# Kernel tuning notes

Hardware: AMD Instinct MI355X
Metric: run time of the kernel (lower is better)

The kernel has to match this reference:

```python
import jax, jax.numpy as jnp
import numpy as np

T, H = 8192, 2048          # num_tokens, hidden_size
NH, NKV, D = 16, 4, 128    # num_heads, num_kv_heads, head_dim
R = 16                     # gate_low_rank_dim
NORM = 16.0                # gate_logit_normalizer
EPS = 1e-6                 # RMSNorm eps


def setup_inputs() -> dict:
    key = jax.random.key(0)
    ks = jax.random.split(key, 8)
    rnd = lambda k, sh, f: jax.random.normal(k, sh, dtype=jnp.float32) * f
    return {
        "hidden_states": rnd(ks[0], (T, H), 1.0),
        "Wqkv": rnd(ks[1], (H, (NH + 2 * NKV) * D), 0.02),
        "bqkv": rnd(ks[2], ((NH + 2 * NKV) * D,), 0.02),
        "gk_w0": rnd(ks[3], (H, R), 0.02),
        "gk_w1": rnd(ks[4], (R, NKV * D), 0.02),
        "gk_b1": rnd(ks[5], (NKV * D,), 0.02),
        "gnorm_w": jnp.ones((D,), jnp.float32),
        "Wo": rnd(ks[6], (NH * D, H), 0.02),
    }


def _gla_scan(q, k, v, g):
    # q,k,v,g: [NH, T, D]. State S: [D, D] per head.
    def step(S, x):
        qt, kt, vt, gt = x
        S = jnp.exp(gt)[:, None] * S + kt[:, None] * vt[None, :]
        return S, qt @ S

    def per_head(qh, kh, vh, gh):
        S0 = jnp.zeros((D, D), qh.dtype)
        _, o = jax.lax.scan(step, S0, (qh, kh, vh, gh))
        return o  # [T, D]

    return jax.vmap(per_head)(q, k, v, g)  # [NH, T, D]


def reference(hidden_states, Wqkv, bqkv, gk_w0, gk_w1, gk_b1, gnorm_w, Wo):
    # qkv projection (with bias), split into q / k / v
    qkv = hidden_states @ Wqkv + bqkv                    # [T, (NH+2*NKV)*D]
    q, k, v = jnp.split(qkv, [NH * D, NH * D + NKV * D], axis=-1)
    # low-rank gate projection (bias0=False, bias1=True)
    gk = (hidden_states @ gk_w0) @ gk_w1 + gk_b1         # [T, NKV*D]

    q = jax.nn.relu(q).reshape(T, NH, D)                 # feature_map = relu
    k = jax.nn.relu(k).reshape(T, NKV, D)
    v = v.reshape(T, NKV, D)
    gk = jax.nn.log_sigmoid(gk).reshape(T, NKV, D) / NORM

    # GQA: repeat_interleave kv heads to NH heads
    rep = NH // NKV
    k = jnp.repeat(k, rep, axis=1)
    v = jnp.repeat(v, rep, axis=1)
    gk = jnp.repeat(gk, rep, axis=1)

    q = q * (D ** -0.5)                                  # fused_chunk_gla default scale

    qh, kh, vh, gh = (t.transpose(1, 0, 2) for t in (q, k, v, gk))  # [NH, T, D]
    o = _gla_scan(qh, kh, vh, gh)                        # [NH, T, D]

    # per-head RMSNorm over head_dim
    o = o * jax.lax.rsqrt(jnp.mean(o * o, axis=-1, keepdims=True) + EPS) * gnorm_w

    o = o.transpose(1, 0, 2).reshape(T, NH * D)          # h n d -> n (h d)
    return o @ Wo                                        # o_proj (no bias)
```

## Files before the change

kernel.cpp:

```cpp
#include <hip/hip_runtime.h>
#include <hip/hip_bf16.h>
#include <cstdint>

typedef unsigned short u16;
typedef unsigned int u32;
typedef float f32x4 __attribute__((ext_vector_type(4)));
typedef short bf16x8 __attribute__((ext_vector_type(8)));

#define T_TOK 8192
#define HID 2048
#define NH 16
#define NKV 4
#define HD 128
#define QKVN 3072
#define CHUNK 64
#define NC 128

__device__ __forceinline__ float bf2f(u16 h){
  u32 u = ((u32)h) << 16;
  return __builtin_bit_cast(float, u);
}
__device__ __forceinline__ u16 f2bf(float f){
  u32 u = __builtin_bit_cast(u32, f);
  u32 r = (u + 0x7fffu + ((u >> 16) & 1u)) >> 16;
  return (u16)r;
}
__device__ __forceinline__ u32 pack2(float a, float b){
  return (u32)f2bf(a) | ((u32)f2bf(b) << 16);
}
__device__ __forceinline__ void gl2lds16(const u16* g, u16* l){
  __builtin_amdgcn_global_load_lds(
      (const __attribute__((address_space(1))) u32*)g,
      (__attribute__((address_space(3))) u32*)l, 16, 0, 0);
}

__global__ __launch_bounds__(256) void cvt_f2b_kernel(
    const float* __restrict__ in, u16* __restrict__ out, int n8)
{
  int i = blockIdx.x*256 + threadIdx.x;
  if (i >= n8) return;
  const float4* p = (const float4*)(in + (size_t)i*8);
  float4 a = p[0], b = p[1];
  uint4 pk;
  pk.x = pack2(a.x, a.y); pk.y = pack2(a.z, a.w);
  pk.z = pack2(b.x, b.y); pk.w = pack2(b.z, b.w);
  *(uint4*)(out + (size_t)i*8) = pk;
}

template<typename YT>
__global__ __launch_bounds__(256) void gemm_m97(
    const u16* __restrict__ X, const u16* __restrict__ Wt,
    const float* __restrict__ bias, const float* __restrict__ ebuf,
    const float* __restrict__ rbuf, YT* __restrict__ Y,
    int M, int N, int K, int mode)
{
  __shared__ u16 As[128*32];
  __shared__ u16 Bs[128*32];
  const int tid = threadIdx.x;
  const int lane = tid & 63;
  const int wave = tid >> 6;
  const int wm = wave >> 1, wn = wave & 1;
  const int bm0 = blockIdx.x * 128, bn0 = blockIdx.y * 128;

  f32x4 acc[4][4];
  #pragma unroll
  for (int i=0;i<4;i++)
    #pragma unroll
    for (int j=0;j<4;j++) acc[i][j] = f32x4{0.f,0.f,0.f,0.f};

  const int row0 = tid >> 2, part8 = (tid & 3) * 8;
  const int mrow = lane & 15, q8 = (lane >> 4) << 3;
  const u16* xb = X  + (size_t)bm0 * K;
  const u16* wb = Wt + (size_t)bn0 * K;

  for (int k0 = 0; k0 < K; k0 += 32) {
    #pragma unroll
    for (int j=0;j<2;j++){
      int rr = j*64 + row0;
      gl2lds16(xb + (size_t)rr*K + k0 + part8, As + rr*32 + part8);
      gl2lds16(wb + (size_t)rr*K + k0 + part8, Bs + rr*32 + part8);
    }
    __syncthreads();
    bf16x8 af[4], bfr[4];
    #pragma unroll
    for (int i=0;i<4;i++){
      af[i]  = *(const bf16x8*)(As + (wm*64 + i*16 + mrow)*32 + q8);
      bfr[i] = *(const bf16x8*)(Bs + (wn*64 + i*16 + mrow)*32 + q8);
    }
    #pragma unroll
    for (int i=0;i<4;i++)
      #pragma unroll
      for (int j=0;j<4;j++)
        acc[i][j] = __builtin_amdgcn_mfma_f32_16x16x32_bf16(af[i], bfr[j], acc[i][j], 0, 0, 0);
    __syncthreads();
  }
  #pragma unroll
  for (int i=0;i<4;i++){
    int row = bm0 + wm*64 + i*16 + (lane>>4)*4;
    #pragma unroll
    for (int j=0;j<4;j++){
      int col = bn0 + wn*64 + j*16 + (lane&15);
      float bv = 0.f;
      if (mode == 1) bv = bias[col];
      #pragma unroll
      for (int rr2=0;rr2<4;rr2++){
        float v = acc[i][j][rr2] + bv;
        if (mode == 1){
          int token = row + rr2;
          int cc = token >> 6, tt = token & 63, ii = col & 127;
          if (col < 2048){
            v = fmaxf(v, 0.f) * 0.08838834764831845f;
            v *= ebuf[(((size_t)cc*4 + (col>>9))*64 + tt)*128 + ii];
          } else if (col < 2560){
            v = fmaxf(v, 0.f);
            v *= rbuf[(((size_t)cc*4 + ((col-2048)>>7))*64 + tt)*128 + ii];
          }
        }
        if (sizeof(YT) == 2) Y[(size_t)(row+rr2)*N + col] = (YT)f2bf(v);
        else                 Y[(size_t)(row+rr2)*N + col] = (YT)v;
      }
    }
  }
}

__global__ __launch_bounds__(256) void transpose_f2b(
    const float* __restrict__ in, u16* __restrict__ out, int R, int C)
{
  __shared__ float tile[32][33];
  int c0 = blockIdx.x*32, r0 = blockIdx.y*32;
  int tx = threadIdx.x & 31, ty = threadIdx.x >> 5;
  #pragma unroll
  for (int p=0;p<4;p++) tile[ty + p*8][tx] = in[(size_t)(r0 + ty + p*8)*C + c0 + tx];
  __syncthreads();
  #pragma unroll
  for (int p=0;p<4;p++) out[(size_t)(c0 + ty + p*8)*R + r0 + tx] = f2bf(tile[tx][ty + p*8]);
}

__global__ __launch_bounds__(256) void gk1_kernel(
    const u16* __restrict__ hsb, const float* __restrict__ w0, float* __restrict__ tmp)
{
  int row = blockIdx.x*4 + (threadIdx.x >> 6);
  int lane = threadIdx.x & 63;
  float acc[16];
  #pragma unroll
  for (int n=0;n<16;n++) acc[n]=0.f;
  for (int k = lane; k < HID; k += 64){
    float h = bf2f(hsb[(size_t)row*HID + k]);
    const float* wr = w0 + (size_t)k*16;
    #pragma unroll
    for (int q=0;q<4;q++){
      float4 wv = *(const float4*)(wr + q*4);
      acc[q*4+0] += h*wv.x; acc[q*4+1] += h*wv.y;
      acc[q*4+2] += h*wv.z; acc[q*4+3] += h*wv.w;
    }
  }
  #pragma unroll
  for (int n=0;n<16;n++){
    #pragma unroll
    for (int off=32; off>0; off>>=1)
      acc[n] += __shfl_down(acc[n], off);
  }
  if (lane == 0){
    #pragma unroll
    for (int n=0;n<16;n++) tmp[(size_t)row*16 + n] = acc[n];
  }
}

__global__ __launch_bounds__(256) void gk2_kernel(
    const float* __restrict__ tmp, const float* __restrict__ w1,
    const float* __restrict__ b1, float* __restrict__ g)
{
  int id = blockIdx.x*256 + threadIdx.x;
  int rrow = id >> 9, n = id & 511;
  float a = b1[n];
  #pragma unroll
  for (int k=0;k<16;k++)
    a += tmp[(size_t)rrow*16 + k] * w1[k*512 + n];
  float ls = fminf(a, 0.f) - log1pf(__expf(-fabsf(a)));
  g[id] = ls * 0.0625f;
}

__global__ __launch_bounds__(256) void decay_kernel(
    const float* __restrict__ g, float* __restrict__ ebuf,
    float* __restrict__ rbuf, float* __restrict__ expB)
{
  __shared__ float bL[CHUNK*HD];
  const int c = blockIdx.x, h = blockIdx.y, tid = threadIdx.x;
  for (int off = tid; off < CHUNK*HD; off += 256){
    int t = off >> 7, i = off & 127;
    bL[off] = g[(size_t)(c*CHUNK + t)*512 + h*HD + i];
  }
  __syncthreads();
  if (tid < HD){
    float run = 0.f;
    for (int t=0;t<CHUNK;t++){ run += bL[t*HD + tid]; bL[t*HD + tid] = run; }
    expB[(size_t)(c*NKV + h)*HD + tid] = __expf(run);
  }
  __syncthreads();
  size_t base = (size_t)(c*NKV + h)*CHUNK*HD;
  for (int off = tid; off < CHUNK*HD; off += 256){
    float b = bL[off];
    ebuf[base + off] = __expf(b);
    rbuf[base + off] = __expf(-b);
  }
}

__global__ __launch_bounds__(256) void chunk_stats2_kernel(
    const u16* __restrict__ qkv, const float* __restrict__ expB,
    u16* __restrict__ Kt, u16* __restrict__ Vt)
{
  __shared__ u16 kL[CHUNK*HD];
  __shared__ u16 vL[CHUNK*HD];
  const int c = blockIdx.x, h = blockIdx.y, tid = threadIdx.x;
  #pragma unroll
  for (int it=0; it<4; it++){
    int u = it*256 + tid;
    int t = u >> 4, p = (u & 15)*8;
    size_t tok = (size_t)(c*CHUNK + t);
    *(uint4*)(kL + t*HD + p) = *(const uint4*)(qkv + tok*QKVN + 2048 + h*HD + p);
    *(uint4*)(vL + t*HD + p) = *(const uint4*)(qkv + tok*QKVN + 2560 + h*HD + p);
  }
  __syncthreads();
  {
    int j = tid >> 1, sh = (tid & 1)*32;
    u16* dst = Vt + ((size_t)(c*NKV + h)*HD + j)*CHUNK + sh;
    #pragma unroll
    for (int s2=0; s2<16; s2++){
      u32 a = (u32)vL[(sh + 2*s2)*HD + j] | ((u32)vL[(sh + 2*s2 + 1)*HD + j] << 16);
      *(u32*)(dst + 2*s2) = a;
    }
  }
  int jj = tid >> 1, ih = (tid & 1)*64;
  float acc[64];
  #pragma unroll
  for (int z=0;z<64;z++) acc[z]=0.f;
  for (int t=0;t<CHUNK;t++){
    float vj = bf2f(vL[t*HD + jj]);
    const u32* kp = (const u32*)(kL + t*HD + ih);
    #pragma unroll
    for (int z2=0; z2<32; z2++){
      u32 kw = kp[z2];
      acc[2*z2]   += vj * bf2f((u16)(kw & 0xffffu));
      acc[2*z2+1] += vj * bf2f((u16)(kw >> 16));
    }
  }
  u16* kout = Kt + ((size_t)(c*NKV + h)*HD + jj)*HD + ih;
  const float* eB = expB + (size_t)(c*NKV + h)*HD + ih;
  #pragma unroll
  for (int z2=0; z2<32; z2++)
    *(u32*)(kout + 2*z2) = pack2(acc[2*z2]*eB[2*z2], acc[2*z2+1]*eB[2*z2+1]);
}

__global__ __launch_bounds__(256) void state_scan2_kernel(
    const u16* __restrict__ Kt, const float* __restrict__ expB, u16* __restrict__ St)
{
  int wid = blockIdx.x;
  int h = wid >> 6;
  int j = (wid & 63)*2 + (threadIdx.x >> 7);
  int i = threadIdx.x & 127;
  size_t base = ((size_t)h*HD + j)*HD + i;
  float S = 0.f;
  for (int cc=0; cc<NC; cc++){
    size_t off = (size_t)cc*(NKV*HD*HD) + base;
    St[off] = f2bf(S);
    S = expB[((size_t)cc*NKV + h)*HD + i] * S + bf2f(Kt[off]);
  }
}

__global__ __launch_bounds__(256) void attn_fused_kernel(
    const u16* __restrict__ qkv, const u16* __restrict__ St,
    const u16* __restrict__ Vt, const float* __restrict__ gw,
    u16* __restrict__ obuf)
{
  __shared__ u16 qe[64*136];
  __shared__ u16 kb[64*136];
  __shared__ u16 sb[64*136];
  __shared__ u16 vb[128*72];
  __shared__ u16 pb[64*72];
  const int c = blockIdx.x, qh = blockIdx.y, h = qh >> 2;
  const int tid = threadIdx.x, lane = tid & 63, w = tid >> 6;
  const int ml = lane & 15, quad = lane >> 4, q8 = quad * 8;

  #pragma unroll
  for (int it = 0; it < 4; it++){
    int u = it*256 + tid;
    int t = u >> 4, p = (u & 15) * 8;
    size_t tok = (size_t)(c*CHUNK + t);
    *(uint4*)(qe + t*136 + p) = *(const uint4*)(qkv + tok*QKVN + qh*HD + p);
    *(uint4*)(kb + t*136 + p) = *(const uint4*)(qkv + tok*QKVN + 2048 + h*HD + p);
  }
  __syncthreads();

  bf16x8 aq[4];
  #pragma unroll
  for (int kk=0;kk<4;kk++)
    aq[kk] = *(const bf16x8*)(qe + (w*16 + ml)*136 + kk*32 + q8);
  #pragma unroll
  for (int n=0;n<4;n++){
    f32x4 pa = {0.f,0.f,0.f,0.f};
    #pragma unroll
    for (int kk=0;kk<4;kk++){
      bf16x8 bk = *(const bf16x8*)(kb + (n*16 + ml)*136 + kk*32 + q8);
      pa = __builtin_amdgcn_mfma_f32_16x16x32_bf16(aq[kk], bk, pa, 0, 0, 0);
    }
    #pragma unroll
    for (int r=0;r<4;r++){
      int ti = quad*4 + r;
      float v = (w*16 + ti >= n*16 + ml) ? pa[r] : 0.f;
      pb[(w*16 + ti)*72 + n*16 + ml] = f2bf(v);
    }
  }
  #pragma unroll
  for (int it = 0; it < 4; it++){
    int u = it*256 + tid;
    int j = u >> 3, p = (u & 7) * 8;
    *(uint4*)(vb + j*72 + p) =
        *(const uint4*)(Vt + ((size_t)(c*NKV + h)*HD + j)*CHUNK + p);
    int t2 = u >> 4, p2 = (u & 15) * 8;
    *(uint4*)(sb + t2*136 + p2) =
        *(const uint4*)(St + ((size_t)(c*NKV + h)*HD + t2)*HD + p2);
  }
  __syncthreads();

  f32x4 o[8];
  #pragma unroll
  for (int n=0;n<8;n++) o[n] = f32x4{0.f,0.f,0.f,0.f};
  bf16x8 ap[2];
  #pragma unroll
  for (int ks=0;ks<2;ks++)
    ap[ks] = *(const bf16x8*)(pb + (w*16 + ml)*72 + ks*32 + q8);
  #pragma unroll
  for (int n=0;n<8;n++)
    #pragma unroll
    for (int ks=0;ks<2;ks++){
      bf16x8 bv = *(const bf16x8*)(vb + (n*16 + ml)*72 + ks*32 + q8);
      o[n] = __builtin_amdgcn_mfma_f32_16x16x32_bf16(ap[ks], bv, o[n], 0, 0, 0);
    }
  #pragma unroll
  for (int n=0;n<4;n++)
    #pragma unroll
    for (int kk=0;kk<4;kk++){
      bf16x8 bs = *(const bf16x8*)(sb + (n*16 + ml)*136 + kk*32 + q8);
      o[n] = __builtin_amdgcn_mfma_f32_16x16x32_bf16(aq[kk], bs, o[n], 0, 0, 0);
    }
  #pragma unroll
  for (int it = 0; it < 4; it++){
    int u = it*256 + tid;
    int t2 = u >> 4, p2 = (u & 15) * 8;
    *(uint4*)(kb + t2*136 + p2) =
        *(const uint4*)(St + ((size_t)(c*NKV + h)*HD + 64 + t2)*HD + p2);
  }
  __syncthreads();
  #pragma unroll
  for (int n=0;n<4;n++)
    #pragma unroll
    for (int kk=0;kk<4;kk++){
      bf16x8 bs = *(const bf16x8*)(kb + (n*16 + ml)*136 + kk*32 + q8);
      o[4+n] = __builtin_amdgcn_mfma_f32_16x16x32_bf16(aq[kk], bs, o[4+n], 0, 0, 0);
    }

  float rstd[4];
  #pragma unroll
  for (int r=0;r<4;r++){
    float s = 0.f;
    #pragma unroll
    for (int n=0;n<8;n++) s += o[n][r]*o[n][r];
    #pragma unroll
    for (int off=1; off<16; off<<=1) s += __shfl_xor(s, off);
    rstd[r] = rsqrtf(s*(1.f/128.f) + 1e-6f);
  }
  #pragma unroll
  for (int n=0;n<8;n++){
    float gwv = gw[n*16 + ml];
    #pragma unroll
    for (int r=0;r<4;r++){
      int t = w*16 + quad*4 + r;
      float val = o[n][r] * rstd[r] * gwv;
      obuf[(size_t)(c*CHUNK + t)*(NH*HD) + qh*HD + n*16 + ml] = f2bf(val);
    }
  }
}

extern "C" void kernel_launch(void* const* d_in, const int* in_sizes, int n_in,
                              void* d_out, int out_size, void* d_ws, size_t ws_size,
                              hipStream_t stream)
{
  const float* hs   = (const float*)d_in[0];
  const float* Wqkv = (const float*)d_in[1];
  const float* bqkv = (const float*)d_in[2];
  const float* w0   = (const float*)d_in[3];
  const float* w1   = (const float*)d_in[4];
  const float* b1   = (const float*)d_in[5];
  const float* gw   = (const float*)d_in[6];
  const float* Wo   = (const float*)d_in[7];
  float* out = (float*)d_out;

  char* ws = (char*)d_ws;
  size_t off = 0;
  auto alloc = [&](size_t bytes)->char*{
    char* p = ws + off; off += (bytes + 255) & ~(size_t)255; return p;
  };
  u16*   hsb   = (u16*)  alloc((size_t)T_TOK*HID*2);
  u16*   Wt1   = (u16*)  alloc((size_t)QKVN*HID*2);
  u16*   Wt2   = (u16*)  alloc((size_t)HID*HID*2);
  u16*   qkv   = (u16*)  alloc((size_t)T_TOK*QKVN*2);
  float* gtmp  = (float*)alloc((size_t)T_TOK*16*4);
  float* g     = (float*)alloc((size_t)T_TOK*512*4);
  float* ebuf  = (float*)alloc((size_t)NC*NKV*CHUNK*HD*4);
  float* rbuf  = (float*)alloc((size_t)NC*NKV*CHUNK*HD*4);
  float* expB  = (float*)alloc((size_t)NC*NKV*HD*4);
  u16*   Kt    = (u16*)  alloc((size_t)NC*NKV*HD*HD*2);
  u16*   St    = (u16*)  alloc((size_t)NC*NKV*HD*HD*2);
  u16*   Vt    = (u16*)  alloc((size_t)NC*NKV*HD*CHUNK*2);
  u16*   obuf  = (u16*)  alloc((size_t)T_TOK*NH*HD*2);

  cvt_f2b_kernel<<<dim3(T_TOK*HID/8/256), 256, 0, stream>>>(hs, hsb, T_TOK*HID/8);
  transpose_f2b<<<dim3(QKVN/32, HID/32), 256, 0, stream>>>(Wqkv, Wt1, HID, QKVN);
  transpose_f2b<<<dim3(HID/32,  HID/32), 256, 0, stream>>>(Wo,   Wt2, HID, HID);
  gk1_kernel<<<dim3(T_TOK/4), 256, 0, stream>>>(hsb, w0, gtmp);
  gk2_kernel<<<dim3(T_TOK*512/256), 256, 0, stream>>>(gtmp, w1, b1, g);
  decay_kernel<<<dim3(NC, NKV), 256, 0, stream>>>(g, ebuf, rbuf, expB);
  gemm_m97<u16><<<dim3(T_TOK/128, QKVN/128), 256, 0, stream>>>(
      hsb, Wt1, bqkv, ebuf, rbuf, qkv, T_TOK, QKVN, HID, 1);
  chunk_stats2_kernel<<<dim3(NC, NKV), 256, 0, stream>>>(qkv, expB, Kt, Vt);
  state_scan2_kernel<<<dim3(256), 256, 0, stream>>>(Kt, expB, St);
  attn_fused_kernel<<<dim3(NC, NH), 256, 0, stream>>>(qkv, St, Vt, gw, obuf);
  gemm_m97<float><<<dim3(T_TOK/128, HID/128), 256, 0, stream>>>(
      obuf, Wt2, nullptr, nullptr, nullptr, out, T_TOK, HID, HID, 0);
}
```

Baseline: 607.1 us.

## Rewrite GEMM with 256x128 tiles, triple-buffered swizzled LDS and XCD-aware mapping

Replaces the simple single-buffered 128x128x32 GEMM with a 512-thread 256x128x64 kernel. Global-to-LDS loads are triple-buffered and issued two tiles ahead, so memory latency overlaps MFMA work. An XOR swizzle in LDS avoids bank conflicts, and setprio raises priority around the MFMA block. Workgroups are remapped so each XCD gets contiguous tiles for better L2 reuse, at the cost of more LDS (144KB) and fragile vmcnt bookkeeping.

New measurement: 599.6 us. About the same (-1.2%).

```diff
diff --git a/kernel.cpp b/kernel.cpp
--- a/kernel.cpp
+++ b/kernel.cpp
@@ -47,63 +47,126 @@
   *(uint4*)(out + (size_t)i*8) = pk;
 }
 
+#define BM 256
+#define BN 128
+#define BK 64
+#define NBUF 3
+#define ABUF (BM*BK)
+#define BBUF (BN*BK)
+#define BUFU (ABUF + BBUF)
+
+__device__ __forceinline__ int swz(int o){ return o ^ (((o >> 7) & 7) << 4); }
+
+__device__ __forceinline__ void stage16(const u16* g, int ldg, u16* l, int o){
+  int p = o ^ (((o >> 7) & 7) << 4);
+  gl2lds16(g + (size_t)(p >> 7) * ldg + ((p >> 1) & 63), l + (o >> 1));
+}
+
 template<typename YT>
-__global__ __launch_bounds__(256) void gemm_m97(
+__global__ __launch_bounds__(512, 2) void gemm_8ph(
     const u16* __restrict__ X, const u16* __restrict__ Wt,
     const float* __restrict__ bias, const float* __restrict__ ebuf,
     const float* __restrict__ rbuf, YT* __restrict__ Y,
     int M, int N, int K, int mode)
 {
-  __shared__ u16 As[128*32];
-  __shared__ u16 Bs[128*32];
-  const int tid = threadIdx.x;
+  __shared__ u16 lds[NBUF * BUFU];
+  const int tid  = threadIdx.x;
   const int lane = tid & 63;
   const int wave = tid >> 6;
-  const int wm = wave >> 1, wn = wave & 1;
-  const int bm0 = blockIdx.x * 128, bn0 = blockIdx.y * 128;
+  const int wm = wave >> 1;
+  const int wn = wave & 1;
+  const int ml = lane & 15, q8 = (lane >> 4) << 3;
+
+  const int MT = M >> 8;
+  const int nwg = gridDim.x;
+  const int q = nwg >> 3, r = nwg & 7;
+  const int xcd = blockIdx.x & 7, loc = blockIdx.x >> 3;
+  const int wg = ((xcd < r) ? xcd * (q + 1) : r * (q + 1) + (xcd - r) * q) + loc;
+  const int bm0 = (wg % MT) * BM;
+  const int bn0 = (wg / MT) * BN;
+
+  const u16* gA = X  + (size_t)bm0 * K;
+  const u16* gB = Wt + (size_t)bn0 * K;
 
   f32x4 acc[4][4];
   #pragma unroll
-  for (int i=0;i<4;i++)
-    #pragma unroll
-    for (int j=0;j<4;j++) acc[i][j] = f32x4{0.f,0.f,0.f,0.f};
-
-  const int row0 = tid >> 2, part8 = (tid & 3) * 8;
-  const int mrow = lane & 15, q8 = (lane >> 4) << 3;
-  const u16* xb = X  + (size_t)bm0 * K;
-  const u16* wb = Wt + (size_t)bn0 * K;
-
-  for (int k0 = 0; k0 < K; k0 += 32) {
-    #pragma unroll
-    for (int j=0;j<2;j++){
-      int rr = j*64 + row0;
-      gl2lds16(xb + (size_t)rr*K + k0 + part8, As + rr*32 + part8);
-      gl2lds16(wb + (size_t)rr*K + k0 + part8, Bs + rr*32 + part8);
-    }
-    __syncthreads();
-    bf16x8 af[4], bfr[4];
-    #pragma unroll
-    for (int i=0;i<4;i++){
-      af[i]  = *(const bf16x8*)(As + (wm*64 + i*16 + mrow)*32 + q8);
-      bfr[i] = *(const bf16x8*)(Bs + (wn*64 + i*16 + mrow)*32 + q8);
-    }
-    #pragma unroll
-    for (int i=0;i<4;i++)
+  for (int i = 0; i < 4; i++)
+    #pragma unroll
+    for (int j = 0; j < 4; j++) acc[i][j] = f32x4{0.f, 0.f, 0.f, 0.f};
+
+  const int NT = K >> 6;
+
+  #pragma unroll
+  for (int t = 0; t < 2; ++t){
+    u16* La = lds + t * BUFU;
+    u16* Lb = La + ABUF;
+    const u16* ga = gA + t * BK;
+    const u16* gb = gB + t * BK;
+    #pragma unroll
+    for (int it = 0; it < 4; ++it) stage16(ga, K, La, (it * 512 + tid) * 16);
+    #pragma unroll
+    for (int it = 0; it < 2; ++it) stage16(gb, K, Lb, (it * 512 + tid) * 16);
+  }
+  asm volatile("s_waitcnt vmcnt(6)" ::: "memory");
+  __syncthreads();
+
+  for (int t = 0; t < NT; ++t){
+    u16* La = lds + (t % NBUF) * BUFU;
+    u16* Lb = La + ABUF;
+    const int ts = t + 2;
+    const bool do_stage = ts < NT;
+    u16* Sa = lds + (ts % NBUF) * BUFU;
+    u16* Sb = Sa + ABUF;
+    const u16* ga = gA + ts * BK;
+    const u16* gb = gB + ts * BK;
+
+    #pragma unroll
+    for (int kk = 0; kk < 2; ++kk){
+      bf16x8 af[4], bfr[4];
       #pragma unroll
-      for (int j=0;j<4;j++)
-        acc[i][j] = __builtin_amdgcn_mfma_f32_16x16x32_bf16(af[i], bfr[j], acc[i][j], 0, 0, 0);
-    __syncthreads();
-  }
-  #pragma unroll
-  for (int i=0;i<4;i++){
-    int row = bm0 + wm*64 + i*16 + (lane>>4)*4;
-    #pragma unroll
-    for (int j=0;j<4;j++){
-      int col = bn0 + wn*64 + j*16 + (lane&15);
+      for (int i = 0; i < 4; ++i){
+        int rowA = wm * 64 + i * 16 + ml;
+        af[i] = *(const bf16x8*)((const char*)La + swz(rowA * 128 + (kk * 32 + q8) * 2));
+      }
+      #pragma unroll
+      for (int j = 0; j < 4; ++j){
+        int rowB = wn * 64 + j * 16 + ml;
+        bfr[j] = *(const bf16x8*)((const char*)Lb + swz(rowB * 128 + (kk * 32 + q8) * 2));
+      }
+      if (do_stage){
+        stage16(ga, K, Sa, ((kk * 2 + 0) * 512 + tid) * 16);
+        stage16(ga, K, Sa, ((kk * 2 + 1) * 512 + tid) * 16);
+        stage16(gb, K, Sb, (kk * 512 + tid) * 16);
+      }
+      __builtin_amdgcn_sched_barrier(0);
+      __builtin_amdgcn_s_barrier();
+      asm volatile("s_waitcnt lgkmcnt(0)" ::: "memory");
+      __builtin_amdgcn_sched_barrier(0);
+      __builtin_amdgcn_s_setprio(1);
+      #pragma unroll
+      for (int i = 0; i < 4; ++i)
+        #pragma unroll
+        for (int j = 0; j < 4; ++j)
+          acc[i][j] = __builtin_amdgcn_mfma_f32_16x16x32_bf16(af[i], bfr[j], acc[i][j], 0, 0, 0);
+      __builtin_amdgcn_s_setprio(0);
+      if (kk == 1){
+        if (ts < NT)         asm volatile("s_waitcnt vmcnt(6)" ::: "memory");
+        else if (t + 1 < NT) asm volatile("s_waitcnt vmcnt(0)" ::: "memory");
+      }
+      __builtin_amdgcn_s_barrier();
+    }
+  }
+
+  #pragma unroll
+  for (int i = 0; i < 4; i++){
+    int row = bm0 + wm * 64 + i * 16 + (lane >> 4) * 4;
+    #pragma unroll
+    for (int j = 0; j < 4; j++){
+      int col = bn0 + wn * 64 + j * 16 + (lane & 15);
       float bv = 0.f;
       if (mode == 1) bv = bias[col];
       #pragma unroll
-      for (int rr2=0;rr2<4;rr2++){
+      for (int rr2 = 0; rr2 < 4; rr2++){
         float v = acc[i][j][rr2] + bv;
         if (mode == 1){
           int token = row + rr2;
@@ -420,11 +483,11 @@
   gk1_kernel<<<dim3(T_TOK/4), 256, 0, stream>>>(hsb, w0, gtmp);
   gk2_kernel<<<dim3(T_TOK*512/256), 256, 0, stream>>>(gtmp, w1, b1, g);
   decay_kernel<<<dim3(NC, NKV), 256, 0, stream>>>(g, ebuf, rbuf, expB);
-  gemm_m97<u16><<<dim3(T_TOK/128, QKVN/128), 256, 0, stream>>>(
+  gemm_8ph<u16><<<dim3((T_TOK/BM)*(QKVN/BN)), 512, 0, stream>>>(
       hsb, Wt1, bqkv, ebuf, rbuf, qkv, T_TOK, QKVN, HID, 1);
   chunk_stats2_kernel<<<dim3(NC, NKV), 256, 0, stream>>>(qkv, expB, Kt, Vt);
   state_scan2_kernel<<<dim3(256), 256, 0, stream>>>(Kt, expB, St);
   attn_fused_kernel<<<dim3(NC, NH), 256, 0, stream>>>(qkv, St, Vt, gw, obuf);
-  gemm_m97<float><<<dim3(T_TOK/128, HID/128), 256, 0, stream>>>(
+  gemm_8ph<float><<<dim3((T_TOK/BM)*(HID/BN)), 512, 0, stream>>>(
       obuf, Wt2, nullptr, nullptr, nullptr, out, T_TOK, HID, HID, 0);
 }
```

## Triple-buffer GEMM LDS loads and remap workgroups across XCDs

Applied to the files above, without the earlier changes.

The GEMM now uses a three-stage LDS ring buffer, issuing async global-to-LDS loads two K-tiles ahead and synchronising with vmcnt waits plus a single barrier per iteration, in place of the load/sync/compute/sync pattern. The grid becomes 1D and block indices are remapped so consecutive logical tiles land on the same XCD (blockIdx mod 8), aiming for better L2 reuse. This raises LDS use to 48KB per block, which may lower occupancy, and it depends on the vmcnt counts being correct.

Result: faster. 581.2 us (-4.3%).

```diff
diff --git a/kernel.cpp b/kernel.cpp
--- a/kernel.cpp
+++ b/kernel.cpp
@@ -48,19 +48,24 @@
 }
 
 template<typename YT>
-__global__ __launch_bounds__(256) void gemm_m97(
+__global__ __launch_bounds__(256) void gemm_v4(
     const u16* __restrict__ X, const u16* __restrict__ Wt,
     const float* __restrict__ bias, const float* __restrict__ ebuf,
     const float* __restrict__ rbuf, YT* __restrict__ Y,
     int M, int N, int K, int mode)
 {
-  __shared__ u16 As[128*32];
-  __shared__ u16 Bs[128*32];
+  __shared__ u16 lds[3 * 8192];
   const int tid = threadIdx.x;
   const int lane = tid & 63;
   const int wave = tid >> 6;
   const int wm = wave >> 1, wn = wave & 1;
-  const int bm0 = blockIdx.x * 128, bn0 = blockIdx.y * 128;
+
+  const int nwg = gridDim.x;
+  const int chunk = nwg >> 3;
+  const int lg = (blockIdx.x & 7) * chunk + (blockIdx.x >> 3);
+  const int NBt = N >> 7;
+  const int bm0 = (lg / NBt) * 128;
+  const int bn0 = (lg % NBt) * 128;
 
   f32x4 acc[4][4];
   #pragma unroll
@@ -73,14 +78,36 @@
   const u16* xb = X  + (size_t)bm0 * K;
   const u16* wb = Wt + (size_t)bn0 * K;
 
-  for (int k0 = 0; k0 < K; k0 += 32) {
+  const int NT = K >> 5;
+
+  #pragma unroll
+  for (int tt = 0; tt < 2; ++tt){
+    u16* As = lds + tt * 8192;
+    u16* Bs = As + 4096;
+    int k0 = tt * 32;
     #pragma unroll
     for (int j=0;j<2;j++){
       int rr = j*64 + row0;
       gl2lds16(xb + (size_t)rr*K + k0 + part8, As + rr*32 + part8);
       gl2lds16(wb + (size_t)rr*K + k0 + part8, Bs + rr*32 + part8);
     }
-    __syncthreads();
+  }
+  asm volatile("s_waitcnt vmcnt(4)" ::: "memory");
+  __builtin_amdgcn_s_barrier();
+
+  for (int t = 0; t < NT; ++t){
+    u16* As = lds + (t % 3) * 8192;
+    u16* Bs = As + 4096;
+    if (t + 2 < NT){
+      u16* Ns = lds + ((t + 2) % 3) * 8192;
+      int k0 = (t + 2) * 32;
+      #pragma unroll
+      for (int j=0;j<2;j++){
+        int rr = j*64 + row0;
+        gl2lds16(xb + (size_t)rr*K + k0 + part8, Ns + rr*32 + part8);
+        gl2lds16(wb + (size_t)rr*K + k0 + part8, Ns + 4096 + rr*32 + part8);
+      }
+    }
     bf16x8 af[4], bfr[4];
     #pragma unroll
     for (int i=0;i<4;i++){
@@ -92,8 +119,11 @@
       #pragma unroll
       for (int j=0;j<4;j++)
         acc[i][j] = __builtin_amdgcn_mfma_f32_16x16x32_bf16(af[i], bfr[j], acc[i][j], 0, 0, 0);
-    __syncthreads();
-  }
+    if (t + 2 < NT)      asm volatile("s_waitcnt vmcnt(4)" ::: "memory");
+    else if (t + 1 < NT) asm volatile("s_waitcnt vmcnt(0)" ::: "memory");
+    __builtin_amdgcn_s_barrier();
+  }
+
   #pragma unroll
   for (int i=0;i<4;i++){
     int row = bm0 + wm*64 + i*16 + (lane>>4)*4;
@@ -420,11 +450,11 @@
   gk1_kernel<<<dim3(T_TOK/4), 256, 0, stream>>>(hsb, w0, gtmp);
   gk2_kernel<<<dim3(T_TOK*512/256), 256, 0, stream>>>(gtmp, w1, b1, g);
   decay_kernel<<<dim3(NC, NKV), 256, 0, stream>>>(g, ebuf, rbuf, expB);
-  gemm_m97<u16><<<dim3(T_TOK/128, QKVN/128), 256, 0, stream>>>(
+  gemm_v4<u16><<<dim3((T_TOK/128)*(QKVN/128)), 256, 0, stream>>>(
       hsb, Wt1, bqkv, ebuf, rbuf, qkv, T_TOK, QKVN, HID, 1);
   chunk_stats2_kernel<<<dim3(NC, NKV), 256, 0, stream>>>(qkv, expB, Kt, Vt);
   state_scan2_kernel<<<dim3(256), 256, 0, stream>>>(Kt, expB, St);
   attn_fused_kernel<<<dim3(NC, NH), 256, 0, stream>>>(qkv, St, Vt, gw, obuf);
-  gemm_m97<float><<<dim3(T_TOK/128, HID/128), 256, 0, stream>>>(
+  gemm_v4<float><<<dim3((T_TOK/128)*(HID/128)), 256, 0, stream>>>(
       obuf, Wt2, nullptr, nullptr, nullptr, out, T_TOK, HID, HID, 0);
 }
```
